# Performance work log

Measured on AMD Instinct MI355X. Metric: run time of the kernel, lower is better.

Reference implementation:

```python
import jax, jax.numpy as jnp
import numpy as np

BITS = 4
MAXQ = (1 << BITS) - 1  # 15
PACK = 32 // BITS       # 8 nibbles per int32


def setup_inputs() -> dict:
    key = jax.random.key(0)
    k = jax.random.split(key, 6)
    B, S, IN, OUT, G = 4, 2048, 4096, 4096, 32
    groups = IN // G  # 128
    imin, imax = np.iinfo(np.int32).min, np.iinfo(np.int32).max
    x = jax.random.normal(k[0], (B, S, IN), dtype=jnp.float32)
    qweight = jax.random.randint(k[1], (IN // PACK, OUT), imin, imax, dtype=jnp.int32)
    qzeros = jax.random.randint(k[2], (groups, OUT // PACK), imin, imax, dtype=jnp.int32)
    qscales = jax.random.randint(k[3], (groups, OUT, 1), 0, 256, dtype=jnp.int32)
    qscales_zeros = jax.random.uniform(k[4], (groups, 1, 1), dtype=jnp.float32)
    qscales_scales = jax.random.uniform(k[5], (groups, 1, 1), dtype=jnp.float32) * 0.01
    g_idx = (jnp.arange(IN, dtype=jnp.int32) // G)
    return {"x": x, "qweight": qweight, "qzeros": qzeros, "qscales": qscales,
            "qscales_zeros": qscales_zeros, "qscales_scales": qscales_scales, "g_idx": g_idx}


def reference(x, qweight, qzeros, qscales, qscales_zeros, qscales_scales, g_idx):
    out_features = qweight.shape[-1]
    shifts = jnp.arange(0, 32, BITS, dtype=jnp.int32)  # (8,)
    # --- unpack int4 weights: (in/8, 8, out) -> (in, out); mask makes arith shift == logical
    w = (qweight[:, None, :] >> shifts[None, :, None]) & MAXQ
    w = w.reshape(-1, out_features)  # (in, out), values 0..15
    # --- unpack zeros: (groups, out/8, 8) -> (groups, out); +1 per original
    z = ((qzeros[:, :, None] >> shifts[None, None, :]) & MAXQ) + 1
    z = z.reshape(qzeros.shape[0], -1)  # (groups, out)
    z = z[g_idx]  # (in, out)
    # --- double-dequant scales: (groups, out, 1) with (groups, 1, 1) stats
    scales = (qscales.astype(x.dtype) - qscales_zeros) * qscales_scales
    scales = scales.reshape(qscales.shape[0], -1)[g_idx]  # (in, out)
    weight = ((w - z) * scales).astype(x.dtype)  # (in, out)
    return jnp.matmul(x, weight)
```

## Files before the change

### kernel.cpp

```cpp
#include <hip/hip_runtime.h>

typedef __attribute__((ext_vector_type(8))) short short8;
typedef __attribute__((ext_vector_type(4))) float floatx4;
typedef __attribute__((ext_vector_type(16))) float f32x16;
typedef unsigned int u32;
typedef unsigned short u16;

__device__ __forceinline__ u16 f2bf(float f) {
  u32 u = __float_as_uint(f);
  u += 0x7FFFu + ((u >> 16) & 1u);
  return (u16)(u >> 16);
}

typedef const __attribute__((address_space(1))) u32* gp1_t;
typedef __attribute__((address_space(3))) u32* lp3_t;

__device__ __forceinline__ void gld16(const void* g, void* l) {
  __builtin_amdgcn_global_load_lds((gp1_t)g, (lp3_t)l, 16, 0, 0);
}

__global__ __launch_bounds__(256) void xconv(const float* __restrict__ x,
                                             u16* __restrict__ xb, long long n4) {
  long long i = (long long)blockIdx.x * 256 + threadIdx.x;
  if (i >= n4) return;
  float4 v = ((const float4*)x)[i];
  ushort4 o;
  o.x = f2bf(v.x); o.y = f2bf(v.y); o.z = f2bf(v.z); o.w = f2bf(v.w);
  ((ushort4*)xb)[i] = o;
}

__global__ __launch_bounds__(256) void dequant(
    const int* __restrict__ qw, const int* __restrict__ qz,
    const int* __restrict__ qs, const float* __restrict__ qsz,
    const float* __restrict__ qss, const int* __restrict__ gidx,
    u16* __restrict__ Wt, int IN, int OUT) {
  const int n = blockIdx.x * 64 + (threadIdx.x & 63);
  const int w = threadIdx.x >> 6;
  const int k0 = blockIdx.y * 128 + w * 32;
  const int g = gidx[k0];
  const int kk0 = k0 >> 3;
  const int zq = ((qz[(size_t)g * (OUT >> 3) + (n >> 3)] >> (4 * (n & 7))) & 15) + 1;
  const float sc = ((float)qs[(size_t)g * OUT + n] - qsz[g]) * qss[g];
  u16* dst = Wt + (size_t)n * IN + k0;
#pragma unroll
  for (int j = 0; j < 4; ++j) {
    const int w32 = qw[(size_t)(kk0 + j) * OUT + n];
    u16 o[8];
#pragma unroll
    for (int s = 0; s < 8; ++s)
      o[s] = f2bf((float)(((w32 >> (4 * s)) & 15) - zq) * sc);
    uint4 pk;
    pk.x = (u32)o[0] | ((u32)o[1] << 16);
    pk.y = (u32)o[2] | ((u32)o[3] << 16);
    pk.z = (u32)o[4] | ((u32)o[5] << 16);
    pk.w = (u32)o[6] | ((u32)o[7] << 16);
    *(uint4*)(dst + j * 8) = pk;
  }
}

#define VM4 asm volatile("s_waitcnt vmcnt(4)" ::: "memory")
#define VM0 asm volatile("s_waitcnt vmcnt(0)" ::: "memory")

__global__ __launch_bounds__(512, 2) void gemm256(const u16* __restrict__ A,
                                                  const u16* __restrict__ Bt,
                                                  float* __restrict__ C,
                                                  int M, int N, int K) {
  __shared__ u16 As[2][16384];
  __shared__ u16 Bs[2][16384];
  const int tid = threadIdx.x;
  const int lane = tid & 63;
  const int wave = tid >> 6;
  const int wm = wave >> 2;
  const int wn = wave & 3;
  const int l31 = lane & 31, hi = lane >> 5, l7 = lane & 7;

  const int nbx = N >> 8;
  const int nwg = gridDim.x;
  const int bid = blockIdx.x;
  const int q8 = nwg >> 3, r8 = nwg & 7;
  const int xcd = bid & 7, loc = bid >> 3;
  const int swz = (xcd < r8 ? xcd * (q8 + 1) : r8 * (q8 + 1) + (xcd - r8) * q8) + loc;
  const int n0 = (swz % nbx) << 8;
  const int m0 = (swz / nbx) << 8;

  f32x16 acc[4][2] = {};

  const int srow = lane >> 3;
  const int sch8 = ((lane & 7) ^ (srow & 7)) * 8;
  const u16* aS = A + (size_t)(m0 + wave * 8 + srow) * K + sch8;
  const u16* bS = Bt + (size_t)(n0 + wave * 8 + srow) * K + sch8;

#define STAGE_A(buf, h, kt) do {                                              \
    const u16* s_ = aS + (size_t)(h) * 128 * K + (size_t)(kt) * 64;           \
    u16* d_ = &As[buf][((h) * 128 + wave * 8) * 64];                          \
    gld16(s_, d_); gld16(s_ + (size_t)64 * K, d_ + 4096);                     \
  } while (0)
#define STAGE_B(buf, h, kt) do {                                              \
    const u16* s_ = bS + (size_t)(h) * 128 * K + (size_t)(kt) * 64;           \
    u16* d_ = &Bs[buf][((h) * 128 + wave * 8) * 64];                          \
    gld16(s_, d_); gld16(s_ + (size_t)64 * K, d_ + 4096);                     \
  } while (0)

  int ko[4];
#pragma unroll
  for (int ks = 0; ks < 4; ++ks) ko[ks] = ((ks * 2 + hi) ^ l7) * 8;
  const u16* a0rd = &As[0][(wm * 128 + l31) * 64];
  const u16* a1rd = &As[1][(wm * 128 + l31) * 64];
  const u16* b0rd = &Bs[0][(wn * 64 + l31) * 64];
  const u16* b1rd = &Bs[1][(wn * 64 + l31) * 64];

  short8 aF[2][4], bF[2][4];

#define PHASE(ARD, BRD, q, LOADB, STG, VMW) do {                              \
    if (LOADB) {                                                              \
      _Pragma("unroll") for (int nt = 0; nt < 2; ++nt)                        \
        _Pragma("unroll") for (int ks = 0; ks < 4; ++ks)                      \
          bF[nt][ks] = *(const short8*)((BRD) + nt * 2048 + ko[ks]);          \
    }                                                                         \
    _Pragma("unroll") for (int j = 0; j < 2; ++j)                             \
      _Pragma("unroll") for (int ks = 0; ks < 4; ++ks)                        \
        aF[j][ks] = *(const short8*)((ARD) + (2 * (q) + j) * 2048 + ko[ks]);  \
    STG;                                                                      \
    __builtin_amdgcn_s_barrier();                                             \
    __builtin_amdgcn_s_setprio(1);                                            \
    _Pragma("unroll") for (int ks = 0; ks < 4; ++ks)                          \
      _Pragma("unroll") for (int j = 0; j < 2; ++j)                           \
        _Pragma("unroll") for (int nt = 0; nt < 2; ++nt)                      \
          acc[2 * (q) + j][nt] = __builtin_amdgcn_mfma_f32_32x32x16_bf16(     \
              aF[j][ks], bF[nt][ks], acc[2 * (q) + j][nt], 0, 0, 0);          \
    __builtin_amdgcn_s_setprio(0);                                            \
    VMW;                                                                      \
    __builtin_amdgcn_s_barrier();                                             \
  } while (0)

  STAGE_B(0, 0, 0); STAGE_B(0, 1, 0);
  STAGE_A(0, 0, 0); STAGE_A(0, 1, 0);
  STAGE_B(1, 0, 1); STAGE_B(1, 1, 1);
  VM4;
  __builtin_amdgcn_s_barrier();

  const int NI = K >> 7;
  for (int i = 0; i < NI; ++i) {
    const int kt = 2 * i;
    const bool full = (i < NI - 1);
    PHASE(a0rd, b0rd, 0, 1, { STAGE_A(1, 0, kt + 1); STAGE_A(1, 1, kt + 1); },
          (void)0);
    PHASE(a0rd, b0rd, 1, 0,
          { if (full) { STAGE_B(0, 0, kt + 2); STAGE_B(0, 1, kt + 2); } },
          { if (full) { VM4; } else { VM0; } });
    PHASE(a1rd, b1rd, 0, 1,
          { if (full) { STAGE_A(0, 0, kt + 2); STAGE_A(0, 1, kt + 2); } },
          (void)0);
    PHASE(a1rd, b1rd, 1, 0,
          { if (full) { STAGE_B(1, 0, kt + 3); STAGE_B(1, 1, kt + 3); } },
          { if (full) { VM4; } });
  }
#undef PHASE
#undef STAGE_A
#undef STAGE_B

#pragma unroll
  for (int mt = 0; mt < 4; ++mt)
#pragma unroll
    for (int nt = 0; nt < 2; ++nt)
#pragma unroll
      for (int r = 0; r < 16; ++r) {
        int row = m0 + wm * 128 + mt * 32 + (r & 3) + 8 * (r >> 2) + 4 * hi;
        int col = n0 + wn * 64 + nt * 32 + l31;
        C[(size_t)row * N + col] = acc[mt][nt][r];
      }
}

__global__ __launch_bounds__(256) void gemm(const u16* __restrict__ A,
                                            const u16* __restrict__ Bt,
                                            float* __restrict__ C,
                                            int M, int N, int K) {
  __shared__ u16 As[128 * 64];
  __shared__ u16 Bs[128 * 64];
  const int tid = threadIdx.x;
  const int lane = tid & 63;
  const int wave = tid >> 6;
  const int wm = wave & 1, wn = wave >> 1;
  const int lr = lane & 15, quad = lane >> 4;
  const int m0 = blockIdx.y * 128, n0 = blockIdx.x * 128;

  floatx4 acc[4][4] = {};

  const int srowB = (lane >> 3);
  const int schunk = (lane & 7) ^ srowB;
  const int rowA0 = wave * 32;
  const u16* aSrc = A + (size_t)(m0 + rowA0 + srowB) * K + schunk * 8;
  const u16* bSrc = Bt + (size_t)(n0 + rowA0 + srowB) * K + schunk * 8;
  u16* aDst = &As[rowA0 * 64];
  u16* bDst = &Bs[rowA0 * 64];
  const size_t rstep = (size_t)8 * K;

  const int rx = lr & 7;

  for (int k0 = 0; k0 < K; k0 += 64) {
    __syncthreads();
#pragma unroll
    for (int c = 0; c < 4; ++c) {
      gld16(aSrc + c * rstep + k0, aDst + c * 8 * 64);
      gld16(bSrc + c * rstep + k0, bDst + c * 8 * 64);
    }
    __syncthreads();

#pragma unroll
    for (int h = 0; h < 2; ++h) {
      short8 aF[4], bF[4];
      const int rc = ((quad + 4 * h) ^ rx) * 8;
#pragma unroll
      for (int t = 0; t < 4; ++t) {
        aF[t] = *(const short8*)&As[(wm * 64 + t * 16 + lr) * 64 + rc];
        bF[t] = *(const short8*)&Bs[(wn * 64 + t * 16 + lr) * 64 + rc];
      }
#pragma unroll
      for (int mt = 0; mt < 4; ++mt)
#pragma unroll
        for (int nt = 0; nt < 4; ++nt)
          acc[mt][nt] = __builtin_amdgcn_mfma_f32_16x16x32_bf16(
              aF[mt], bF[nt], acc[mt][nt], 0, 0, 0);
    }
  }

#pragma unroll
  for (int mt = 0; mt < 4; ++mt)
#pragma unroll
    for (int nt = 0; nt < 4; ++nt)
#pragma unroll
      for (int r = 0; r < 4; ++r) {
        int row = m0 + wm * 64 + mt * 16 + quad * 4 + r;
        int col = n0 + wn * 64 + nt * 16 + lr;
        C[(size_t)row * N + col] = acc[mt][nt][r];
      }
}

__global__ void naive(const float* __restrict__ x, const int* __restrict__ qw,
                      const int* __restrict__ qz, const int* __restrict__ qs,
                      const float* __restrict__ qsz, const float* __restrict__ qss,
                      const int* __restrict__ gidx, float* __restrict__ out,
                      int M, int N, int K) {
  int n = blockIdx.x * 64 + (threadIdx.x & 63);
  int m = blockIdx.y * 4 + (threadIdx.x >> 6);
  if (n >= N || m >= M) return;
  float acc = 0.f;
  for (int kk = 0; kk < K / 8; ++kk) {
    int w32 = qw[(size_t)kk * N + n];
#pragma unroll
    for (int s = 0; s < 8; ++s) {
      int k = kk * 8 + s;
      int g = gidx[k];
      int zq = ((qz[(size_t)g * (N >> 3) + (n >> 3)] >> (4 * (n & 7))) & 15) + 1;
      float sc = ((float)qs[(size_t)g * N + n] - qsz[g]) * qss[g];
      acc += x[(size_t)m * K + k] * ((float)((w32 >> (4 * s)) & 15) - (float)zq) * sc;
    }
  }
  out[(size_t)m * N + n] = acc;
}

extern "C" void kernel_launch(void* const* d_in, const int* in_sizes, int n_in,
                              void* d_out, int out_size, void* d_ws, size_t ws_size,
                              hipStream_t stream) {
  const float* x = (const float*)d_in[0];
  const int* qw = (const int*)d_in[1];
  const int* qz = (const int*)d_in[2];
  const int* qs = (const int*)d_in[3];
  const float* qsz = (const float*)d_in[4];
  const float* qss = (const float*)d_in[5];
  const int* gidx = (const int*)d_in[6];
  const int IN = in_sizes[6];
  const int OUT = (int)(((long long)in_sizes[1] * 8) / IN);
  const int M = in_sizes[0] / IN;
  float* out = (float*)d_out;

  size_t bytesW = (size_t)IN * OUT * 2;
  size_t bytesX = (size_t)M * IN * 2;
  bool haveWs = (ws_size >= bytesW + bytesX);
  bool fast256 = haveWs && (M % 256 == 0) && (OUT % 256 == 0) &&
                 (IN % 128 == 0) && (IN >= 256);
  bool fast128 = haveWs && (M % 128 == 0) && (OUT % 128 == 0) && (IN % 128 == 0);

  if (fast256 || fast128) {
    u16* Wt = (u16*)d_ws;
    u16* Xb = (u16*)((char*)d_ws + bytesW);
    long long n4 = (long long)M * IN / 4;
    int cb = (int)((n4 + 255) / 256);
    xconv<<<cb, 256, 0, stream>>>(x, Xb, n4);
    dequant<<<dim3(OUT / 64, IN / 128), 256, 0, stream>>>(qw, qz, qs, qsz, qss,
                                                          gidx, Wt, IN, OUT);
    if (fast256) {
      int nblk = (M / 256) * (OUT / 256);
      gemm256<<<dim3(nblk), 512, 0, stream>>>(Xb, Wt, out, M, OUT, IN);
    } else {
      gemm<<<dim3(OUT / 128, M / 128), 256, 0, stream>>>(Xb, Wt, out, M, OUT, IN);
    }
  } else {
    naive<<<dim3((OUT + 63) / 64, (M + 3) / 4), 256, 0, stream>>>(
        x, qw, qz, qs, qsz, qss, gidx, out, M, OUT, IN);
  }
}
```

Before: 512.5 us.

## Split GEMM LDS tiles into k-halves and stage dequant output through LDS

The GEMM's LDS tiles are reorganized into two 32-wide k sub-buffers per stage, with a new XOR swizzle and a staging pattern where each wave loads 16 rows of 4 16-byte chunks. This aims to improve global-load coalescing per row and reduce LDS bank conflicts on fragment reads. The dequant kernel now writes unpacked bf16 values into a shared tile and then stores full contiguous 64-byte row segments, so the transposed weight writes are better coalesced. The cost is added LDS use and a barrier in dequant, plus more complex addressing in the GEMM.

Result: no change. 512.0 us (-0.1%).

```diff
diff --git a/kernel.cpp b/kernel.cpp
--- a/kernel.cpp
+++ b/kernel.cpp
@@ -34,27 +34,41 @@
     const int* __restrict__ qs, const float* __restrict__ qsz,
     const float* __restrict__ qss, const int* __restrict__ gidx,
     u16* __restrict__ Wt, int IN, int OUT) {
-  const int n = blockIdx.x * 64 + (threadIdx.x & 63);
-  const int w = threadIdx.x >> 6;
-  const int k0 = blockIdx.y * 128 + w * 32;
-  const int g = gidx[k0];
-  const int kk0 = k0 >> 3;
-  const int zq = ((qz[(size_t)g * (OUT >> 3) + (n >> 3)] >> (4 * (n & 7))) & 15) + 1;
-  const float sc = ((float)qs[(size_t)g * OUT + n] - qsz[g]) * qss[g];
-  u16* dst = Wt + (size_t)n * IN + k0;
-#pragma unroll
-  for (int j = 0; j < 4; ++j) {
-    const int w32 = qw[(size_t)(kk0 + j) * OUT + n];
-    u16 o[8];
-#pragma unroll
-    for (int s = 0; s < 8; ++s)
-      o[s] = f2bf((float)(((w32 >> (4 * s)) & 15) - zq) * sc);
-    uint4 pk;
-    pk.x = (u32)o[0] | ((u32)o[1] << 16);
-    pk.y = (u32)o[2] | ((u32)o[3] << 16);
-    pk.z = (u32)o[4] | ((u32)o[5] << 16);
-    pk.w = (u32)o[6] | ((u32)o[7] << 16);
-    *(uint4*)(dst + j * 8) = pk;
+  __shared__ u16 Lt[64][136];
+  const int t = threadIdx.x;
+  const int n0 = blockIdx.x * 64;
+  const int k0 = blockIdx.y * 128;
+
+  {
+    const int nl = t & 63, kw = t >> 6;
+    const int n = n0 + nl;
+#pragma unroll
+    for (int j = 0; j < 4; ++j) {
+      const int widx = kw + j * 4;
+      const int g = gidx[k0 + widx * 8];
+      const int zq = ((qz[(size_t)g * (OUT >> 3) + (n >> 3)] >> (4 * (n & 7))) & 15) + 1;
+      const float sc = ((float)qs[(size_t)g * OUT + n] - qsz[g]) * qss[g];
+      const int w32 = qw[(size_t)(k0 / 8 + widx) * OUT + n];
+      u16 o[8];
+#pragma unroll
+      for (int s = 0; s < 8; ++s)
+        o[s] = f2bf((float)(((w32 >> (4 * s)) & 15) - zq) * sc);
+      uint4 pk;
+      pk.x = (u32)o[0] | ((u32)o[1] << 16);
+      pk.y = (u32)o[2] | ((u32)o[3] << 16);
+      pk.z = (u32)o[4] | ((u32)o[5] << 16);
+      pk.w = (u32)o[6] | ((u32)o[7] << 16);
+      *(uint4*)&Lt[nl][widx * 8] = pk;
+    }
+  }
+  __syncthreads();
+
+  {
+    const int nl = t >> 2, kq = t & 3;
+    u16* dst = Wt + (size_t)(n0 + nl) * IN + k0 + kq * 32;
+#pragma unroll
+    for (int i = 0; i < 4; ++i)
+      *(uint4*)(dst + i * 8) = *(const uint4*)&Lt[nl][kq * 32 + i * 8];
   }
 }
 
@@ -65,14 +79,14 @@
                                                   const u16* __restrict__ Bt,
                                                   float* __restrict__ C,
                                                   int M, int N, int K) {
-  __shared__ u16 As[2][16384];
-  __shared__ u16 Bs[2][16384];
+  __shared__ u16 As[2][2][8192];
+  __shared__ u16 Bs[2][2][8192];
   const int tid = threadIdx.x;
   const int lane = tid & 63;
   const int wave = tid >> 6;
   const int wm = wave >> 2;
   const int wn = wave & 3;
-  const int l31 = lane & 31, hi = lane >> 5, l7 = lane & 7;
+  const int l31 = lane & 31, hi = lane >> 5;
 
   const int nbx = N >> 8;
   const int nwg = gridDim.x;
@@ -85,41 +99,47 @@
 
   f32x16 acc[4][2] = {};
 
-  const int srow = lane >> 3;
-  const int sch8 = ((lane & 7) ^ (srow & 7)) * 8;
-  const u16* aS = A + (size_t)(m0 + wave * 8 + srow) * K + sch8;
-  const u16* bS = Bt + (size_t)(n0 + wave * 8 + srow) * K + sch8;
-
-#define STAGE_A(buf, h, kt) do {                                              \
-    const u16* s_ = aS + (size_t)(h) * 128 * K + (size_t)(kt) * 64;           \
-    u16* d_ = &As[buf][((h) * 128 + wave * 8) * 64];                          \
-    gld16(s_, d_); gld16(s_ + (size_t)64 * K, d_ + 4096);                     \
+  const int srow = lane >> 2;
+  const int sg = ((lane & 3) ^ ((lane >> 3) & 3)) * 8;
+  const u16* aS = A + (size_t)(m0 + wave * 16 + srow) * K + sg;
+  const u16* bS = Bt + (size_t)(n0 + wave * 16 + srow) * K + sg;
+
+#define STAGE_A(buf, kt) do {                                                 \
+    _Pragma("unroll") for (int h_ = 0; h_ < 2; ++h_)                          \
+      _Pragma("unroll") for (int sb_ = 0; sb_ < 2; ++sb_)                     \
+        gld16(aS + (size_t)h_ * 128 * K + (size_t)(kt) * 64 + sb_ * 32,       \
+              &As[buf][sb_][(h_ * 128 + wave * 16) * 32]);                    \
   } while (0)
-#define STAGE_B(buf, h, kt) do {                                              \
-    const u16* s_ = bS + (size_t)(h) * 128 * K + (size_t)(kt) * 64;           \
-    u16* d_ = &Bs[buf][((h) * 128 + wave * 8) * 64];                          \
-    gld16(s_, d_); gld16(s_ + (size_t)64 * K, d_ + 4096);                     \
+#define STAGE_B(buf, kt) do {                                                 \
+    _Pragma("unroll") for (int h_ = 0; h_ < 2; ++h_)                          \
+      _Pragma("unroll") for (int sb_ = 0; sb_ < 2; ++sb_)                     \
+        gld16(bS + (size_t)h_ * 128 * K + (size_t)(kt) * 64 + sb_ * 32,       \
+              &Bs[buf][sb_][(h_ * 128 + wave * 16) * 32]);                    \
   } while (0)
 
+  const int rsw = (l31 >> 1) & 3;
   int ko[4];
 #pragma unroll
-  for (int ks = 0; ks < 4; ++ks) ko[ks] = ((ks * 2 + hi) ^ l7) * 8;
-  const u16* a0rd = &As[0][(wm * 128 + l31) * 64];
-  const u16* a1rd = &As[1][(wm * 128 + l31) * 64];
-  const u16* b0rd = &Bs[0][(wn * 64 + l31) * 64];
-  const u16* b1rd = &Bs[1][(wn * 64 + l31) * 64];
+  for (int ks = 0; ks < 4; ++ks) ko[ks] = ((((ks & 1) * 2 + hi)) ^ rsw) * 8;
+  const u32 aBase = (u32)(wm * 128 + l31) * 32;
+  const u32 bBase = (u32)(wn * 64 + l31) * 32;
+  const u16* a0p[2] = { &As[0][0][aBase], &As[0][1][aBase] };
+  const u16* a1p[2] = { &As[1][0][aBase], &As[1][1][aBase] };
+  const u16* b0p[2] = { &Bs[0][0][bBase], &Bs[0][1][bBase] };
+  const u16* b1p[2] = { &Bs[1][0][bBase], &Bs[1][1][bBase] };
 
   short8 aF[2][4], bF[2][4];
 
-#define PHASE(ARD, BRD, q, LOADB, STG, VMW) do {                              \
+#define PHASE(AP, BP, q, LOADB, STG, VMW) do {                                \
     if (LOADB) {                                                              \
       _Pragma("unroll") for (int nt = 0; nt < 2; ++nt)                        \
         _Pragma("unroll") for (int ks = 0; ks < 4; ++ks)                      \
-          bF[nt][ks] = *(const short8*)((BRD) + nt * 2048 + ko[ks]);          \
+          bF[nt][ks] = *(const short8*)(BP[ks >> 1] + nt * 1024 + ko[ks]);    \
     }                                                                         \
     _Pragma("unroll") for (int j = 0; j < 2; ++j)                             \
       _Pragma("unroll") for (int ks = 0; ks < 4; ++ks)                        \
-        aF[j][ks] = *(const short8*)((ARD) + (2 * (q) + j) * 2048 + ko[ks]);  \
+        aF[j][ks] =                                                           \
+            *(const short8*)(AP[ks >> 1] + (2 * (q) + j) * 1024 + ko[ks]);    \
     STG;                                                                      \
     __builtin_amdgcn_s_barrier();                                             \
     __builtin_amdgcn_s_setprio(1);                                            \
@@ -133,9 +153,9 @@
     __builtin_amdgcn_s_barrier();                                             \
   } while (0)
 
-  STAGE_B(0, 0, 0); STAGE_B(0, 1, 0);
-  STAGE_A(0, 0, 0); STAGE_A(0, 1, 0);
-  STAGE_B(1, 0, 1); STAGE_B(1, 1, 1);
+  STAGE_B(0, 0);
+  STAGE_A(0, 0);
+  STAGE_B(1, 1);
   VM4;
   __builtin_amdgcn_s_barrier();
 
@@ -143,16 +163,11 @@
   for (int i = 0; i < NI; ++i) {
     const int kt = 2 * i;
     const bool full = (i < NI - 1);
-    PHASE(a0rd, b0rd, 0, 1, { STAGE_A(1, 0, kt + 1); STAGE_A(1, 1, kt + 1); },
-          (void)0);
-    PHASE(a0rd, b0rd, 1, 0,
-          { if (full) { STAGE_B(0, 0, kt + 2); STAGE_B(0, 1, kt + 2); } },
+    PHASE(a0p, b0p, 0, 1, { STAGE_A(1, kt + 1); }, (void)0);
+    PHASE(a0p, b0p, 1, 0, { if (full) STAGE_B(0, kt + 2); },
           { if (full) { VM4; } else { VM0; } });
-    PHASE(a1rd, b1rd, 0, 1,
-          { if (full) { STAGE_A(0, 0, kt + 2); STAGE_A(0, 1, kt + 2); } },
-          (void)0);
-    PHASE(a1rd, b1rd, 1, 0,
-          { if (full) { STAGE_B(1, 0, kt + 3); STAGE_B(1, 1, kt + 3); } },
+    PHASE(a1p, b1p, 0, 1, { if (full) STAGE_A(0, kt + 2); }, (void)0);
+    PHASE(a1p, b1p, 1, 0, { if (full) STAGE_B(1, kt + 3); },
           { if (full) { VM4; } });
   }
 #undef PHASE
```
